# Kernel optimization log

Hardware: AMD Instinct MI355X
Metric: run time of the kernel (lower is better)

Reference implementation:

```python
import jax, jax.numpy as jnp
import numpy as np

OUT = 7          # pooler output_size
RATIO = 2        # sampling_ratio
MIN_LEVEL, MAX_LEVEL = 2, 5
CANON_SIZE, CANON_LEVEL = 224.0, 4.0
SCALES = (0.25, 0.125, 0.0625, 0.03125)


def setup_inputs() -> dict:
    key = jax.random.key(0)
    ks = jax.random.split(key, 8)
    feat2 = jax.random.normal(ks[0], (2, 256, 200, 304), dtype=jnp.float32)
    feat3 = jax.random.normal(ks[1], (2, 256, 100, 152), dtype=jnp.float32)
    feat4 = jax.random.normal(ks[2], (2, 256, 50, 76), dtype=jnp.float32)
    feat5 = jax.random.normal(ks[3], (2, 256, 25, 38), dtype=jnp.float32)
    M = 1000
    imH, imW = 800.0, 1216.0
    cx = jax.random.uniform(ks[4], (M,)) * imW
    cy = jax.random.uniform(ks[5], (M,)) * imH
    wh = jax.random.uniform(ks[6], (M, 2)) * 400.0 + 8.0  # box sizes 8..408 px -> spans levels 2..5
    x0 = jnp.clip(cx - wh[:, 0] / 2, 0.0, imW - 1.0)
    x1 = jnp.clip(cx + wh[:, 0] / 2, 1.0, imW)
    y0 = jnp.clip(cy - wh[:, 1] / 2, 0.0, imH - 1.0)
    y1 = jnp.clip(cy + wh[:, 1] / 2, 1.0, imH)
    boxes = jnp.stack([x0, y0, x1, y1], axis=1).astype(jnp.float32)
    batch_idx = jax.random.randint(ks[7], (M,), 0, 2, dtype=jnp.int32)
    return {"feat2": feat2, "feat3": feat3, "feat4": feat4, "feat5": feat5,
            "boxes": boxes, "batch_idx": batch_idx}


def _assign_levels(boxes):
    # detectron2 assign_boxes_to_levels
    area = (boxes[:, 2] - boxes[:, 0]) * (boxes[:, 3] - boxes[:, 1])
    size = jnp.sqrt(area)
    lvl = jnp.floor(CANON_LEVEL + jnp.log2(size / CANON_SIZE + 1e-8))
    lvl = jnp.clip(lvl, MIN_LEVEL, MAX_LEVEL)
    return (lvl - MIN_LEVEL).astype(jnp.int32)  # [M] in 0..3


def _axis_weights(c, size):
    # torchvision roi_align bilinear clamping (per axis, separable)
    valid = ((c >= -1.0) & (c <= size)).astype(c.dtype)
    cc = jnp.maximum(c, 0.0)
    lo_f = jnp.floor(cc)
    cap = lo_f >= size - 1
    lo = jnp.where(cap, size - 1, lo_f).astype(jnp.int32)
    hi = jnp.where(cap, size - 1, lo + 1).astype(jnp.int32)
    l = jnp.where(cap, 0.0, cc - lo_f)
    return lo, hi, (1.0 - l) * valid, l * valid


def _roi_align(feat, boxes, bidx, scale):
    # feat [N,C,H,W], boxes [M,4] xyxy, aligned=True (ROIAlignV2)
    N, C, H, W = feat.shape
    M = boxes.shape[0]
    b = boxes * scale - 0.5  # aligned: shift by -0.5 after scaling
    x0, y0 = b[:, 0], b[:, 1]
    bin_w = (b[:, 2] - x0) / OUT
    bin_h = (b[:, 3] - y0) / OUT
    S = OUT * RATIO
    s = np.arange(S)
    offs = jnp.asarray((s // RATIO) + ((s % RATIO) + 0.5) / RATIO, dtype=feat.dtype)  # [S]
    ys = y0[:, None] + bin_h[:, None] * offs[None, :]  # [M,S]
    xs = x0[:, None] + bin_w[:, None] * offs[None, :]  # [M,S]
    ylo, yhi, wyl, wyh = _axis_weights(ys, H)
    xlo, xhi, wxl, wxh = _axis_weights(xs, W)

    def gather(yi, xi):
        # -> [M, S, S, C]
        return feat[bidx[:, None, None], :, yi[:, :, None], xi[:, None, :]]

    val = (gather(ylo, xlo) * (wyl[:, :, None] * wxl[:, None, :])[..., None]
         + gather(ylo, xhi) * (wyl[:, :, None] * wxh[:, None, :])[..., None]
         + gather(yhi, xlo) * (wyh[:, :, None] * wxl[:, None, :])[..., None]
         + gather(yhi, xhi) * (wyh[:, :, None] * wxh[:, None, :])[..., None])
    # average over the RATIOxRATIO sample subgrid of each output bin
    val = val.reshape(M, OUT, RATIO, OUT, RATIO, C).mean(axis=(2, 4))
    return val.transpose(0, 3, 1, 2)  # [M, C, OUT, OUT]


def reference(feat2, feat3, feat4, feat5, boxes, batch_idx):
    feats = (feat2, feat3, feat4, feat5)
    assign = _assign_levels(boxes)  # [M]
    M, C = boxes.shape[0], feat2.shape[1]
    out = jnp.zeros((M, C, OUT, OUT), dtype=feat2.dtype)
    for lvl, (f, sc) in enumerate(zip(feats, SCALES)):
        pooled = _roi_align(f, boxes, batch_idx, sc)
        out = out + pooled * (assign == lvl)[:, None, None, None].astype(out.dtype)
    return out
```

## Files before the change

kernel.cpp:

```cpp
#include <hip/hip_runtime.h>


#define NCH 256
#define POOL 7
#define NBIN 49
#define CAP 1152
#define WPB 4
#define TS 128

typedef __attribute__((address_space(3))) void       as3_void;
typedef __attribute__((address_space(1))) const void as1_void;

__global__ __launch_bounds__(256) void roi_precompute_kernel(
    const float* __restrict__ boxes, const int* __restrict__ bidx,
    unsigned int* __restrict__ tab, int M)
{
    const int lane = threadIdx.x & 63;
    const int m = blockIdx.x * WPB + (threadIdx.x >> 6);
    if (m >= M) return;

    float bx0 = boxes[4 * m + 0];
    float by0 = boxes[4 * m + 1];
    float bx1 = boxes[4 * m + 2];
    float by1 = boxes[4 * m + 3];

    float area = (bx1 - bx0) * (by1 - by0);
    float sz   = sqrtf(area);
    float lvlf = floorf(4.0f + log2f(sz / 224.0f + 1e-8f));
    lvlf = fminf(fmaxf(lvlf, 2.0f), 5.0f);
    int lvl = (int)lvlf - 2;

    int H, W; float scale;
    if (lvl == 0)      { H = 200; W = 304; scale = 0.25f;    }
    else if (lvl == 1) { H = 100; W = 152; scale = 0.125f;   }
    else if (lvl == 2) { H = 50;  W = 76;  scale = 0.0625f;  }
    else               { H = 25;  W = 38;  scale = 0.03125f; }

    float x0 = bx0 * scale - 0.5f;
    float y0 = by0 * scale - 0.5f;
    float bin_w = (bx1 * scale - 0.5f - x0) * (1.0f / 7.0f);
    float bin_h = (by1 * scale - 0.5f - y0) * (1.0f / 7.0f);

    int axis = lane >= 14;
    int s    = axis ? (lane - 14) : lane;
    float off = (float)(s >> 1) + ((s & 1) ? 0.75f : 0.25f);
    float cv    = axis ? (y0 + bin_h * off) : (x0 + bin_w * off);
    float size  = axis ? (float)H : (float)W;
    float valid = (cv >= -1.0f && cv <= size) ? 1.0f : 0.0f;
    float cc    = fmaxf(cv, 0.0f);
    float lo_f  = floorf(cc);
    bool  capd  = lo_f >= size - 1.0f;
    int   lo    = capd ? (int)size - 1 : (int)lo_f;
    int   hi    = capd ? lo : lo + 1;
    float l     = capd ? 0.0f : (cc - lo_f);
    float wlo   = (1.0f - l) * valid;
    float whi   = l * valid;

    int rx0 = __shfl(lo, 0);
    int rxe = __shfl(hi, 13);
    int ry0 = __shfl(lo, 14);
    int rye = __shfl(hi, 27);

    int FW  = rxe - rx0 + 1;
    int FH  = rye - ry0 + 1;
    int lpr = (FW + 3) >> 2;
    int RS4 = lpr << 2;
    int rpi = 64 / lpr;
    int iters = (FH + rpi - 1) / rpi;
    unsigned Mg  = (65536u   + (unsigned)lpr - 1u) / (unsigned)lpr;
    unsigned Mg2 = (4194304u + (unsigned)RS4 - 1u) / (unsigned)RS4;
    unsigned HW  = (unsigned)(H * W);
    unsigned base_off = (unsigned)bidx[m] * 256u * HW
                      + (unsigned)ry0 * (unsigned)W + (unsigned)rx0;
    int FH2 = FH;
    if (FH2 * RS4 > CAP) FH2 = CAP / RS4;
    unsigned lastoff = base_off + 255u * HW
                     + (unsigned)(FH - 1) * (unsigned)W + (unsigned)RS4;
    int safe = (lastoff <= 2u * 256u * HW) && (FH * RS4 <= CAP);

    unsigned* t = tab + (size_t)m * TS;
    if (lane == 0) {
        t[0]  = base_off;
        t[1]  = (unsigned)lvl;
        t[2]  = HW;
        t[3]  = (unsigned)W;
        t[4]  = (unsigned)lpr;
        t[5]  = Mg;
        t[6]  = (unsigned)rpi;
        t[7]  = (unsigned)iters;
        t[8]  = (unsigned)(rpi * W);
        t[9]  = (unsigned)((rpi * RS4) << 2);
        t[10] = (unsigned)((FH - 1) * W);
        t[11] = (unsigned)safe;
        t[12] = (unsigned)FW;
        t[13] = (unsigned)RS4;
        t[14] = (unsigned)FH2;
        t[15] = Mg2;
    }
    if (lane < 28) {
        if (!axis) {
            int xr = lo - rx0;
            int xp = min(xr + 1, FW - 1);
            uint4 v;
            v.x = (unsigned)xr;
            v.y = (unsigned)xp;
            v.z = __float_as_uint(wlo);
            v.w = __float_as_uint(whi);
            *(uint4*)(t + 16 + 4 * s) = v;
        } else {
            uint4 v;
            v.x = (unsigned)((lo - ry0) * RS4);
            v.y = (unsigned)((hi - ry0) * RS4);
            v.z = __float_as_uint(wlo);
            v.w = __float_as_uint(whi);
            *(uint4*)(t + 72 + 4 * s) = v;
        }
    }
}

__global__ __launch_bounds__(256, 8) void roi_align_kernel(
    const float* __restrict__ f0, const float* __restrict__ f1,
    const float* __restrict__ f2, const float* __restrict__ f3,
    const unsigned int* __restrict__ tab,
    float* __restrict__ out, int M)
{
    __shared__ float sF[WPB][CAP];

    const int lane = threadIdx.x & 63;
    const int w    = __builtin_amdgcn_readfirstlane(threadIdx.x >> 6);

    const unsigned mblocks = (unsigned)gridDim.x >> 8;
    const unsigned rb   = blockIdx.x;
    const unsigned xcd  = rb & 7u;
    const unsigned idx  = rb >> 3;
    const unsigned cblk = idx / mblocks;
    const unsigned mb   = idx - cblk * mblocks;
    const int c = (int)(xcd * 32u + cblk);
    const int m = (int)(mb * WPB) + w;
    if (m >= M) return;
    const int unit = m * NCH + c;

    const unsigned* t = tab + (size_t)m * TS;

    const int ci = lane < NBIN ? lane : 0;
    const int py = ci / POOL;
    const int px = ci - POOL * py;
    const uint4* xt = (const uint4*)(t + 16);
    const uint4* yt = (const uint4*)(t + 72);
    const uint4 X0 = xt[2 * px];
    const uint4 X1 = xt[2 * px + 1];
    const uint4 Y0 = yt[2 * py];
    const uint4 Y1 = yt[2 * py + 1];

    const uint4 s0 = *(const uint4*)(t);
    const uint4 s1 = *(const uint4*)(t + 4);
    const uint4 s2 = *(const uint4*)(t + 8);

    const int lvl = __builtin_amdgcn_readfirstlane((int)s0.y);
    const float* fp = (lvl == 0) ? f0 : (lvl == 1) ? f1 : (lvl == 2) ? f2 : f3;
    const unsigned HW = s0.z;
    const unsigned Wd = s0.w;
    const float* src = fp + (size_t)(s0.x + (unsigned)c * HW);

    const int safe = __builtin_amdgcn_readfirstlane((int)s2.w);
    if (safe) {
        const int lpr      = __builtin_amdgcn_readfirstlane((int)s1.x);
        const unsigned Mg  = s1.y;
        const int rpi      = __builtin_amdgcn_readfirstlane((int)s1.z);
        const int iters    = __builtin_amdgcn_readfirstlane((int)s1.w);
        const unsigned gstep  = s2.x;
        const unsigned lstepB = __builtin_amdgcn_readfirstlane((int)s2.y);
        const unsigned fhw    = s2.z;

        int sfy  = (int)(((unsigned)lane * Mg) >> 16);
        int sfx4 = (lane - sfy * lpr) << 2;
        if (sfy < rpi) {
            const float* g    = src + (unsigned)sfy * Wd + (unsigned)sfx4;
            const float* gmax = src + fhw + (unsigned)sfx4;
            char* lb = (char*)&sF[w][0];
            for (int it = 0; it < iters; ++it) {
                const float* gc = (g > gmax) ? gmax : g;
                __builtin_amdgcn_global_load_lds((as1_void*)gc,
                                                 (as3_void*)lb, 16, 0, 0);
                g  += gstep;
                lb += lstepB;
            }
        }
    } else {
        const uint4 s3 = *(const uint4*)(t + 12);
        const int FW  = __builtin_amdgcn_readfirstlane((int)s3.x);
        const int RS4 = __builtin_amdgcn_readfirstlane((int)s3.y);
        const int FH2 = __builtin_amdgcn_readfirstlane((int)s3.z);
        const unsigned Mg2 = s3.w;
        const int tot = FH2 * RS4;
        for (int i = lane; i < tot; i += 64) {
            int fy = (int)(((unsigned)i * Mg2) >> 22);
            int fx = i - fy * RS4;
            int cx = fx < FW ? fx : FW - 1;
            sF[w][i] = src[(unsigned)fy * Wd + (unsigned)cx];
        }
    }

    __builtin_amdgcn_s_waitcnt(0);
    __asm__ __volatile__("" ::: "memory");

    if (lane < NBIN) {
        const float* Fb = &sF[w][0];
        const unsigned xr0 = X0.x, xp0 = X0.y, xr1 = X1.x, xp1 = X1.y;
        const float wxl0 = __uint_as_float(X0.z), wxh0 = __uint_as_float(X0.w);
        const float wxl1 = __uint_as_float(X1.z), wxh1 = __uint_as_float(X1.w);
        const unsigned ra = Y0.x, rb2 = Y0.y, rc = Y1.x, rd = Y1.y;

        float a0 = Fb[ra + xr0] * wxl0 + Fb[ra + xp0] * wxh0
                 + Fb[ra + xr1] * wxl1 + Fb[ra + xp1] * wxh1;
        float a1 = Fb[rb2 + xr0] * wxl0 + Fb[rb2 + xp0] * wxh0
                 + Fb[rb2 + xr1] * wxl1 + Fb[rb2 + xp1] * wxh1;
        float a2 = Fb[rc + xr0] * wxl0 + Fb[rc + xp0] * wxh0
                 + Fb[rc + xr1] * wxl1 + Fb[rc + xp1] * wxh1;
        float a3 = Fb[rd + xr0] * wxl0 + Fb[rd + xp0] * wxh0
                 + Fb[rd + xr1] * wxl1 + Fb[rd + xp1] * wxh1;

        float acc = __uint_as_float(Y0.z) * a0 + __uint_as_float(Y0.w) * a1
                  + __uint_as_float(Y1.z) * a2 + __uint_as_float(Y1.w) * a3;

        out[(size_t)unit * NBIN + lane] = acc * 0.25f;
    }
}

extern "C" void kernel_launch(void* const* d_in, const int* in_sizes, int n_in,
                              void* d_out, int out_size, void* d_ws, size_t ws_size,
                              hipStream_t stream) {
    const float* f0    = (const float*)d_in[0];
    const float* f1    = (const float*)d_in[1];
    const float* f2    = (const float*)d_in[2];
    const float* f3    = (const float*)d_in[3];
    const float* boxes = (const float*)d_in[4];
    const int*   bidx  = (const int*)d_in[5];
    float* out = (float*)d_out;

    int M = in_sizes[4] / 4;
    unsigned int* tab = (unsigned int*)d_ws;

    int pblocks = (M + WPB - 1) / WPB;
    hipLaunchKernelGGL(roi_precompute_kernel, dim3(pblocks), dim3(256), 0,
                       stream, boxes, bidx, tab, M);

    int mblocks = (M + WPB - 1) / WPB;
    int blocks = mblocks * NCH;
    hipLaunchKernelGGL(roi_align_kernel, dim3(blocks), dim3(256), 0, stream,
                       f0, f1, f2, f3, tab, out, M);
}
```

Baseline: 281.2 us.

## Process four channels per wave with split async loads overlapping bilinear compute

Each wave now handles four consecutive channels of one ROI rather than one. The global-to-LDS loads are split into two halves: the second half runs a fixed ITMAX-unrolled loop with dummy LDS targets, so a partial vmcnt wait can start bilinear math on the first two channels while the last two are still loading. Blocks shrink to two waves with a larger per-wave LDS buffer. The safe-path criterion is tightened to iters<=ITMAX, which pushes more ROIs onto the slow scalar fallback and uses far more LDS per block, so fewer waves can be resident.

Measured after the change: 285.1 us. No clear change (+1.4%).

```diff
diff --git a/kernel.cpp b/kernel.cpp
--- a/kernel.cpp
+++ b/kernel.cpp
@@ -5,8 +5,12 @@
 #define POOL 7
 #define NBIN 49
 #define CAP 1152
-#define WPB 4
+#define WPB 2
+#define PWPB 4
 #define TS 128
+#define ITMAX 5
+#define UPW 4
+#define DUMPF (UPW * CAP)
 
 typedef __attribute__((address_space(3))) void       as3_void;
 typedef __attribute__((address_space(1))) const void as1_void;
@@ -16,7 +20,7 @@
     unsigned int* __restrict__ tab, int M)
 {
     const int lane = threadIdx.x & 63;
-    const int m = blockIdx.x * WPB + (threadIdx.x >> 6);
+    const int m = blockIdx.x * PWPB + (threadIdx.x >> 6);
     if (m >= M) return;
 
     float bx0 = boxes[4 * m + 0];
@@ -76,7 +80,9 @@
     if (FH2 * RS4 > CAP) FH2 = CAP / RS4;
     unsigned lastoff = base_off + 255u * HW
                      + (unsigned)(FH - 1) * (unsigned)W + (unsigned)RS4;
-    int safe = (lastoff <= 2u * 256u * HW) && (FH * RS4 <= CAP);
+    int safe = (lastoff <= 2u * 256u * HW)
+            && (iters * rpi * RS4 <= CAP)
+            && (iters <= ITMAX);
 
     unsigned* t = tab + (size_t)m * TS;
     if (lane == 0) {
@@ -118,27 +124,38 @@
     }
 }
 
-__global__ __launch_bounds__(256, 8) void roi_align_kernel(
+#define BILIN(Fb, ACC) do {                                                 \
+    float a0_ = Fb[ra + xr0] * wxl0 + Fb[ra + xp0] * wxh0                   \
+              + Fb[ra + xr1] * wxl1 + Fb[ra + xp1] * wxh1;                  \
+    float a1_ = Fb[rb2 + xr0] * wxl0 + Fb[rb2 + xp0] * wxh0                 \
+              + Fb[rb2 + xr1] * wxl1 + Fb[rb2 + xp1] * wxh1;                \
+    float a2_ = Fb[rc + xr0] * wxl0 + Fb[rc + xp0] * wxh0                   \
+              + Fb[rc + xr1] * wxl1 + Fb[rc + xp1] * wxh1;                  \
+    float a3_ = Fb[rd + xr0] * wxl0 + Fb[rd + xp0] * wxh0                   \
+              + Fb[rd + xr1] * wxl1 + Fb[rd + xp1] * wxh1;                  \
+    ACC = wy0 * a0_ + wy1 * a1_ + wy2 * a2_ + wy3 * a3_;                    \
+} while (0)
+
+__global__ __launch_bounds__(128, 2) void roi_align_kernel(
     const float* __restrict__ f0, const float* __restrict__ f1,
     const float* __restrict__ f2, const float* __restrict__ f3,
     const unsigned int* __restrict__ tab,
     float* __restrict__ out, int M)
 {
-    __shared__ float sF[WPB][CAP];
+    __shared__ float sF[WPB][UPW * CAP + 256];
 
     const int lane = threadIdx.x & 63;
     const int w    = __builtin_amdgcn_readfirstlane(threadIdx.x >> 6);
 
-    const unsigned mblocks = (unsigned)gridDim.x >> 8;
+    const unsigned mblocks = (unsigned)gridDim.x >> 6;
     const unsigned rb   = blockIdx.x;
     const unsigned xcd  = rb & 7u;
     const unsigned idx  = rb >> 3;
-    const unsigned cblk = idx / mblocks;
-    const unsigned mb   = idx - cblk * mblocks;
-    const int c = (int)(xcd * 32u + cblk);
-    const int m = (int)(mb * WPB) + w;
+    const unsigned qblk = idx / mblocks;
+    const unsigned mb   = idx - qblk * mblocks;
+    const int c0 = (int)((xcd * 8u + qblk) * 4u);
+    const int m  = (int)(mb * WPB) + w;
     if (m >= M) return;
-    const int unit = m * NCH + c;
 
     const unsigned* t = tab + (size_t)m * TS;
 
@@ -160,7 +177,20 @@
     const float* fp = (lvl == 0) ? f0 : (lvl == 1) ? f1 : (lvl == 2) ? f2 : f3;
     const unsigned HW = s0.z;
     const unsigned Wd = s0.w;
-    const float* src = fp + (size_t)(s0.x + (unsigned)c * HW);
+    const float* src0 = fp + (size_t)(s0.x + (unsigned)c0 * HW);
+
+    const unsigned xr0 = X0.x, xp0 = X0.y, xr1 = X1.x, xp1 = X1.y;
+    const float wxl0 = __uint_as_float(X0.z), wxh0 = __uint_as_float(X0.w);
+    const float wxl1 = __uint_as_float(X1.z), wxh1 = __uint_as_float(X1.w);
+    const unsigned ra = Y0.x, rb2 = Y0.y, rc = Y1.x, rd = Y1.y;
+    const float wy0 = __uint_as_float(Y0.z), wy1 = __uint_as_float(Y0.w);
+    const float wy2 = __uint_as_float(Y1.z), wy3 = __uint_as_float(Y1.w);
+
+    const float* Fb0 = &sF[w][0];
+    const float* Fb1 = &sF[w][CAP];
+    const float* Fb2 = &sF[w][2 * CAP];
+    const float* Fb3 = &sF[w][3 * CAP];
+    float acc0, acc1, acc2, acc3;
 
     const int safe = __builtin_amdgcn_readfirstlane((int)s2.w);
     if (safe) {
@@ -174,18 +204,61 @@
 
         int sfy  = (int)(((unsigned)lane * Mg) >> 16);
         int sfx4 = (lane - sfy * lpr) << 2;
-        if (sfy < rpi) {
-            const float* g    = src + (unsigned)sfy * Wd + (unsigned)sfx4;
-            const float* gmax = src + fhw + (unsigned)sfx4;
-            char* lb = (char*)&sF[w][0];
+        const unsigned lo0 = (unsigned)sfy * Wd + (unsigned)sfx4;
+        const unsigned hi0 = fhw + (unsigned)sfx4;
+        const bool act = sfy < rpi;
+
+        if (act) {
+            const float* gA  = src0 + lo0;
+            const float* gB  = src0 + HW + lo0;
+            const float* gmA = src0 + hi0;
+            const float* gmB = src0 + HW + hi0;
+            char* lA = (char*)Fb0;
+            char* lB = (char*)Fb1;
             for (int it = 0; it < iters; ++it) {
-                const float* gc = (g > gmax) ? gmax : g;
-                __builtin_amdgcn_global_load_lds((as1_void*)gc,
-                                                 (as3_void*)lb, 16, 0, 0);
-                g  += gstep;
-                lb += lstepB;
+                const float* pa = (gA > gmA) ? gmA : gA;
+                const float* pb = (gB > gmB) ? gmB : gB;
+                __builtin_amdgcn_global_load_lds((as1_void*)pa,
+                                                 (as3_void*)lA, 16, 0, 0);
+                __builtin_amdgcn_global_load_lds((as1_void*)pb,
+                                                 (as3_void*)lB, 16, 0, 0);
+                gA += gstep; gB += gstep; lA += lstepB; lB += lstepB;
             }
         }
+        __builtin_amdgcn_sched_barrier(0);
+        if (act) {
+            const float* gC  = src0 + 2u * HW + lo0;
+            const float* gD  = src0 + 3u * HW + lo0;
+            const float* gmC = src0 + 2u * HW + hi0;
+            const float* gmD = src0 + 3u * HW + hi0;
+            char* lC = (char*)Fb2;
+            char* lD = (char*)Fb3;
+            char* dmp = (char*)&sF[w][DUMPF];
+            #pragma unroll
+            for (int it = 0; it < ITMAX; ++it) {
+                const float* pc = (gC > gmC) ? gmC : gC;
+                const float* pd = (gD > gmD) ? gmD : gD;
+                char* wc = (it < iters) ? lC : dmp;
+                char* wd = (it < iters) ? lD : dmp;
+                __builtin_amdgcn_global_load_lds((as1_void*)pc,
+                                                 (as3_void*)wc, 16, 0, 0);
+                __builtin_amdgcn_global_load_lds((as1_void*)pd,
+                                                 (as3_void*)wd, 16, 0, 0);
+                gC += gstep; gD += gstep; lC += lstepB; lD += lstepB;
+            }
+        }
+        static_assert(2 * ITMAX == 10, "update vmcnt immediate");
+        asm volatile("s_waitcnt vmcnt(10)" ::: "memory");
+        __builtin_amdgcn_sched_barrier(0);
+
+        BILIN(Fb0, acc0);
+        BILIN(Fb1, acc1);
+
+        asm volatile("s_waitcnt vmcnt(0)" ::: "memory");
+        __builtin_amdgcn_sched_barrier(0);
+
+        BILIN(Fb2, acc2);
+        BILIN(Fb3, acc3);
     } else {
         const uint4 s3 = *(const uint4*)(t + 12);
         const int FW  = __builtin_amdgcn_readfirstlane((int)s3.x);
@@ -197,33 +270,26 @@
             int fy = (int)(((unsigned)i * Mg2) >> 22);
             int fx = i - fy * RS4;
             int cx = fx < FW ? fx : FW - 1;
-            sF[w][i] = src[(unsigned)fy * Wd + (unsigned)cx];
+            unsigned goff = (unsigned)fy * Wd + (unsigned)cx;
+            sF[w][i]           = src0[goff];
+            sF[w][CAP + i]     = src0[HW + goff];
+            sF[w][2 * CAP + i] = src0[2u * HW + goff];
+            sF[w][3 * CAP + i] = src0[3u * HW + goff];
         }
+        __builtin_amdgcn_s_waitcnt(0);
+        __asm__ __volatile__("" ::: "memory");
+        BILIN(Fb0, acc0);
+        BILIN(Fb1, acc1);
+        BILIN(Fb2, acc2);
+        BILIN(Fb3, acc3);
     }
 
-    __builtin_amdgcn_s_waitcnt(0);
-    __asm__ __volatile__("" ::: "memory");
-
     if (lane < NBIN) {
-        const float* Fb = &sF[w][0];
-        const unsigned xr0 = X0.x, xp0 = X0.y, xr1 = X1.x, xp1 = X1.y;
-        const float wxl0 = __uint_as_float(X0.z), wxh0 = __uint_as_float(X0.w);
-        const float wxl1 = __uint_as_float(X1.z), wxh1 = __uint_as_float(X1.w);
-        const unsigned ra = Y0.x, rb2 = Y0.y, rc = Y1.x, rd = Y1.y;
-
-        float a0 = Fb[ra + xr0] * wxl0 + Fb[ra + xp0] * wxh0
-                 + Fb[ra + xr1] * wxl1 + Fb[ra + xp1] * wxh1;
-        float a1 = Fb[rb2 + xr0] * wxl0 + Fb[rb2 + xp0] * wxh0
-                 + Fb[rb2 + xr1] * wxl1 + Fb[rb2 + xp1] * wxh1;
-        float a2 = Fb[rc + xr0] * wxl0 + Fb[rc + xp0] * wxh0
-                 + Fb[rc + xr1] * wxl1 + Fb[rc + xp1] * wxh1;
-        float a3 = Fb[rd + xr0] * wxl0 + Fb[rd + xp0] * wxh0
-                 + Fb[rd + xr1] * wxl1 + Fb[rd + xp1] * wxh1;
-
-        float acc = __uint_as_float(Y0.z) * a0 + __uint_as_float(Y0.w) * a1
-                  + __uint_as_float(Y1.z) * a2 + __uint_as_float(Y1.w) * a3;
-
-        out[(size_t)unit * NBIN + lane] = acc * 0.25f;
+        size_t ob = ((size_t)m * NCH + (unsigned)c0) * NBIN + (unsigned)lane;
+        out[ob]            = acc0 * 0.25f;
+        out[ob + NBIN]     = acc1 * 0.25f;
+        out[ob + 2 * NBIN] = acc2 * 0.25f;
+        out[ob + 3 * NBIN] = acc3 * 0.25f;
     }
 }
 
@@ -241,12 +307,12 @@
     int M = in_sizes[4] / 4;
     unsigned int* tab = (unsigned int*)d_ws;
 
-    int pblocks = (M + WPB - 1) / WPB;
+    int pblocks = (M + PWPB - 1) / PWPB;
     hipLaunchKernelGGL(roi_precompute_kernel, dim3(pblocks), dim3(256), 0,
                        stream, boxes, bidx, tab, M);
 
     int mblocks = (M + WPB - 1) / WPB;
-    int blocks = mblocks * NCH;
-    hipLaunchKernelGGL(roi_align_kernel, dim3(blocks), dim3(256), 0, stream,
+    int blocks = mblocks * (NCH / UPW);
+    hipLaunchKernelGGL(roi_align_kernel, dim3(blocks), dim3(128), 0, stream,
                        f0, f1, f2, f3, tab, out, M);
 }
```
